# Optimization experiments

Measured on AMD Instinct MI355X. Metric: run time of the kernel, lower is better.

Reference implementation:

```python
import jax, jax.numpy as jnp
import numpy as np

NUM_HEADS = 8
EPS = 1e-5


def setup_inputs() -> dict:
    key = jax.random.key(0)
    ks = jax.random.split(key, 7)
    B, C, H, W, D = 1, 256, 16, 16, 16
    return {
        "x": jax.random.normal(ks[0], (B, C, H, W, D), dtype=jnp.float32),
        "w_dw": jax.random.normal(ks[1], (C, 1, 3, 3, 3), dtype=jnp.float32) * 0.05,
        "b_dw": jax.random.normal(ks[2], (C,), dtype=jnp.float32) * 0.05,
        "w_qkv": jax.random.normal(ks[3], (3 * C, C), dtype=jnp.float32) * 0.05,
        "b_qkv": jax.random.normal(ks[4], (3 * C,), dtype=jnp.float32) * 0.05,
        "w_proj": jax.random.normal(ks[5], (C, C), dtype=jnp.float32) * 0.05,
        "b_proj": jax.random.normal(ks[6], (C,), dtype=jnp.float32) * 0.05,
    }


def reference(x, w_dw, b_dw, w_qkv, b_qkv, w_proj, b_proj):
    B, C, H, W, D = x.shape
    nh = NUM_HEADS
    hd = C // nh
    scale = hd ** (-0.5)
    N = H * W * D

    # depthwise 3x3x3 conv (groups=C), SAME padding
    y = jax.lax.conv_general_dilated(
        x, w_dw, window_strides=(1, 1, 1), padding="SAME",
        dimension_numbers=("NCHWD", "OIHWD", "NCHWD"),
        feature_group_count=C,
    ) + b_dw[None, :, None, None, None]

    # InstanceNorm3d (affine=False): normalize over spatial dims per (b, c)
    mu = y.mean(axis=(2, 3, 4), keepdims=True)
    var = y.var(axis=(2, 3, 4), keepdims=True)
    y = (y - mu) * jax.lax.rsqrt(var + EPS)

    # 1x1x1 conv -> 3*C channels
    qkv = jnp.einsum("bchwd,oc->bohwd", y, w_qkv) + b_qkv[None, :, None, None, None]

    # [B, 3, nh, hd, N] -> q, k, v each [B, nh, N, hd]
    qkv = qkv.reshape(B, 3, nh, hd, N)
    q, k, v = jnp.transpose(qkv, (1, 0, 2, 4, 3))

    attn = jax.nn.softmax(jnp.einsum("bhnd,bhmd->bhnm", q, k) * scale, axis=-1)
    out = jnp.einsum("bhnm,bhmd->bhnd", attn, v)  # [B, nh, N, hd]

    # transpose(-1, -2) then reshape to [B, C, H, W, D]
    out = jnp.transpose(out, (0, 1, 3, 2)).reshape(B, C, H, W, D)

    # output 1x1x1 projection
    out = jnp.einsum("bchwd,oc->bohwd", out, w_proj) + b_proj[None, :, None, None, None]
    return out
```

## Files before the change

### kernel.cpp

```cpp
#include <hip/hip_runtime.h>
#include <hip/hip_bf16.h>

#define NSP 4096
#define QSC2 0.25503486f

typedef __attribute__((ext_vector_type(8))) short bf16x8;
typedef __attribute__((ext_vector_type(4))) float f32x4;
typedef __attribute__((ext_vector_type(16))) float f32x16;

__device__ __forceinline__ unsigned short f2bf(float f){
  union{float f;unsigned int u;}c; c.f=f;
  unsigned int r = c.u + 0x7fffu + ((c.u>>16)&1u);
  return (unsigned short)(r>>16);
}
__device__ __forceinline__ unsigned int pk2(float a, float b){
  __hip_bfloat162 p = __float22bfloat162_rn(make_float2(a, b));
  unsigned int r; __builtin_memcpy(&r, &p, 4); return r;
}
__device__ __forceinline__ ushort4 pk4(float a, float b, float c, float d){
  union { ushort4 u4; uint2 u2; } u;
  u.u2.x = pk2(a, b); u.u2.y = pk2(c, d);
  return u.u4;
}
__device__ __forceinline__ float bfu2f(unsigned short u){
  union { unsigned int i; float f; } c; c.i = ((unsigned int)u) << 16; return c.f;
}

__global__ __launch_bounds__(512) void k_dwconv(
    const float* __restrict__ x,
    const float* __restrict__ wdw,
    const float* __restrict__ bdw,
    unsigned short* __restrict__ ybn)
{
  const int c = blockIdx.x;
  const int tid = threadIdx.x;
  __shared__ float xs[4096];
  __shared__ float wsh[27];
  __shared__ float bsh;
  __shared__ float rs[8], rq[8];

  const float* xc = x + (size_t)c * NSP;
  for (int i = tid; i < 1024; i += 512) *(float4*)&xs[i*4] = ((const float4*)xc)[i];
  if (tid < 27) wsh[tid] = wdw[c*27 + tid];
  if (tid == 31) bsh = bdw[c];
  __syncthreads();

  float yv[8];
  float sum = 0.f, sumsq = 0.f;
  #pragma unroll
  for (int i = 0; i < 8; i++){
    const int n = (i << 9) + tid;
    const int h = n >> 8, w = (n >> 4) & 15, d = n & 15;
    float acc = bsh;
    #pragma unroll
    for (int kh = 0; kh < 3; kh++){
      const int hh = h + kh - 1;
      if ((unsigned)hh >= 16u) continue;
      #pragma unroll
      for (int kw = 0; kw < 3; kw++){
        const int ww = w + kw - 1;
        if ((unsigned)ww >= 16u) continue;
        #pragma unroll
        for (int kd = 0; kd < 3; kd++){
          const int dd = d + kd - 1;
          if ((unsigned)dd >= 16u) continue;
          acc += wsh[kh*9 + kw*3 + kd] * xs[(hh<<8) + (ww<<4) + dd];
        }
      }
    }
    yv[i] = acc; sum += acc; sumsq += acc*acc;
  }
  #pragma unroll
  for (int off = 32; off > 0; off >>= 1){
    sum   += __shfl_down(sum, off, 64);
    sumsq += __shfl_down(sumsq, off, 64);
  }
  const int wid = tid >> 6, lane = tid & 63;
  if (lane == 0){ rs[wid] = sum; rq[wid] = sumsq; }
  __syncthreads();
  float ts = 0.f, tq = 0.f;
  #pragma unroll
  for (int i = 0; i < 8; i++){ ts += rs[i]; tq += rq[i]; }
  const float mean = ts * (1.f/4096.f);
  const float var  = tq * (1.f/4096.f) - mean*mean;
  const float rinv = rsqrtf(var + 1e-5f);
  unsigned short* yo = ybn + (size_t)c * NSP;
  #pragma unroll
  for (int i = 0; i < 8; i++) yo[(i<<9) + tid] = f2bf((yv[i] - mean) * rinv);
}

__global__ __launch_bounds__(256) void k_trans(
    const unsigned short* __restrict__ ybn,
    unsigned short* __restrict__ ynT)
{
  __shared__ unsigned short T[64][72];
  const int tid = threadIdx.x;
  const int n0 = blockIdx.x * 64, c0 = blockIdx.y * 64;
  const int cl = tid >> 4, n4 = (tid & 15) * 4;
  #pragma unroll
  for (int i = 0; i < 4; i++){
    const int c = cl + i*16;
    const ushort4 v = *(const ushort4*)(ybn + (size_t)(c0 + c) * NSP + n0 + n4);
    T[n4+0][c] = v.x; T[n4+1][c] = v.y; T[n4+2][c] = v.z; T[n4+3][c] = v.w;
  }
  __syncthreads();
  const int nl = tid >> 2, s8 = (tid & 3) * 16;
  *(uint4*)(ynT + (size_t)(n0+nl)*256 + c0 + s8)     = *(const uint4*)&T[nl][s8];
  *(uint4*)(ynT + (size_t)(n0+nl)*256 + c0 + s8 + 8) = *(const uint4*)&T[nl][s8 + 8];
}

__global__ __launch_bounds__(256) void k_qkv(
    const float* __restrict__ wqkv,
    const float* __restrict__ bqkv,
    const unsigned short* __restrict__ ynT,
    unsigned short* __restrict__ qb, unsigned short* __restrict__ kb,
    unsigned short* __restrict__ vbt)
{
  __shared__ unsigned short Wb[64][264];
  const int tid = threadIdx.x;
  const int o0 = blockIdx.y * 64;
  const int n0 = blockIdx.x * 64;
  {
    const int row = tid & 63, part = tid >> 6;
    const float* src = wqkv + (size_t)(o0 + row) * 256 + part * 64;
    unsigned short* dst = &Wb[row][part*64];
    #pragma unroll
    for (int j = 0; j < 8; j++){
      const float4 a = ((const float4*)src)[2*j];
      const float4 b = ((const float4*)src)[2*j+1];
      *(ushort4*)&dst[j*8]     = pk4(a.x, a.y, a.z, a.w);
      *(ushort4*)&dst[j*8 + 4] = pk4(b.x, b.y, b.z, b.w);
    }
  }
  __syncthreads();

  const int w = tid >> 6, lane = tid & 63, quad = lane >> 4, cc = lane & 15;
  const int nbase = n0 + w*16;
  const bool isv = (o0 >= 512);
  f32x4 acc[4] = {};

  #pragma unroll
  for (int k = 0; k < 8; k++){
    const bf16x8 y0 = *(const bf16x8*)(ynT + (size_t)(nbase + cc) * 256 + k*32 + quad*8);
    #pragma unroll
    for (int os = 0; os < 4; os++){
      const bf16x8 wf = *(const bf16x8*)&Wb[os*16 + cc][k*32 + quad*8];
      if (!isv) acc[os] = __builtin_amdgcn_mfma_f32_16x16x32_bf16(y0, wf, acc[os], 0, 0, 0);
      else      acc[os] = __builtin_amdgcn_mfma_f32_16x16x32_bf16(wf, y0, acc[os], 0, 0, 0);
    }
  }

  if (!isv){
    #pragma unroll
    for (int os = 0; os < 4; os++){
      const int o = o0 + os*16 + cc;
      const int g = o >> 8, hh = (o >> 5) & 7, dd = o & 31;
      const float bias = bqkv[o];
      const float sc = (g == 0) ? QSC2 : 1.f;
      unsigned short* dst = (g == 0) ? qb : kb;
      #pragma unroll
      for (int r = 0; r < 4; r++){
        const int n = nbase + quad*4 + r;
        dst[((size_t)hh * NSP + n) * 32 + dd] = f2bf((acc[os][r] + bias) * sc);
      }
    }
  } else {
    #pragma unroll
    for (int os = 0; os < 4; os++){
      #pragma unroll
      for (int r = 0; r < 4; r++){
        const int orow = o0 - 512 + os*16 + quad*4 + r;
        const float bias = bqkv[512 + orow];
        const int n = nbase + cc;
        vbt[(size_t)orow * NSP + n] = f2bf(acc[os][r] + bias);
      }
    }
  }
}

__global__ __launch_bounds__(256) void k_attn(
    const unsigned short* __restrict__ qb,
    const unsigned short* __restrict__ kb,
    const unsigned short* __restrict__ vbt,
    unsigned short* __restrict__ opb, float* __restrict__ lp, int ktlen)
{
  const int h = blockIdx.y, q0 = blockIdx.x * 128, z = blockIdx.z;
  const int tid = threadIdx.x;
  const int w = tid >> 6, l = tid & 63;
  const int lq = l & 31, lb = l >> 5;

  __shared__ unsigned short ks [64][40];
  __shared__ unsigned short vsT[32][72];
  __shared__ unsigned short pst[128][72];

  const int qg = q0 + w*32 + lq;
  const bf16x8 qf0 = *(const bf16x8*)(qb + ((size_t)(h*NSP + qg))*32 + lb*8);
  const bf16x8 qf1 = *(const bf16x8*)(qb + ((size_t)(h*NSP + qg))*32 + 16 + lb*8);
  const unsigned short* kbase = kb  + (size_t)h * NSP * 32;
  const unsigned short* vbase = vbt + (size_t)h * 32 * NSP;

  f32x16 oacc = {};
  float lsum = 0.f;

  const int kt0 = z * ktlen;
  const int krow = tid >> 2, kseg = (tid & 3) * 8;
  const int vrow = tid >> 3, vseg = (tid & 7) * 8;
  const int iters = ktlen >> 6;

  for (int it = 0; it < iters; it++){
    const int kt = kt0 + it * 64;
    {
      *(uint4*)&ks[krow][kseg]  = *(const uint4*)(kbase + (size_t)(kt + krow) * 32 + kseg);
      *(uint4*)&vsT[vrow][vseg] = *(const uint4*)(vbase + (size_t)vrow * NSP + kt + vseg);
    }
    __syncthreads();

    #pragma unroll
    for (int t2 = 0; t2 < 2; t2++){
      const bf16x8 af0 = *(const bf16x8*)&ks[t2*32 + lq][lb*8];
      const bf16x8 af1 = *(const bf16x8*)&ks[t2*32 + lq][16 + lb*8];
      f32x16 sa = {};
      sa = __builtin_amdgcn_mfma_f32_32x32x16_bf16(af0, qf0, sa, 0, 0, 0);
      sa = __builtin_amdgcn_mfma_f32_32x32x16_bf16(af1, qf1, sa, 0, 0, 0);
      #pragma unroll
      for (int g = 0; g < 4; g++){
        const float p0 = __builtin_amdgcn_exp2f(sa[g*4+0]);
        const float p1 = __builtin_amdgcn_exp2f(sa[g*4+1]);
        const float p2 = __builtin_amdgcn_exp2f(sa[g*4+2]);
        const float p3 = __builtin_amdgcn_exp2f(sa[g*4+3]);
        lsum += (p0 + p1) + (p2 + p3);
        *(ushort4*)&pst[w*32 + lq][t2*32 + g*8 + lb*4] = pk4(p0, p1, p2, p3);
      }
    }
    #pragma unroll
    for (int ck = 0; ck < 4; ck++){
      const bf16x8 vf = *(const bf16x8*)&vsT[lq]       [ck*16 + lb*8];
      const bf16x8 pf = *(const bf16x8*)&pst[w*32 + lq][ck*16 + lb*8];
      oacc = __builtin_amdgcn_mfma_f32_32x32x16_bf16(vf, pf, oacc, 0, 0, 0);
    }
    __syncthreads();
  }

  lsum += __shfl_xor(lsum, 32, 64);

  unsigned short* dst = opb + ((size_t)z * NSP + qg) * 256 + h*32;
  #pragma unroll
  for (int g = 0; g < 4; g++){
    *(ushort4*)(dst + g*8 + lb*4) =
        pk4(oacc[g*4+0], oacc[g*4+1], oacc[g*4+2], oacc[g*4+3]);
  }
  if (lb == 0) lp[((size_t)z * 8 + h) * NSP + qg] = lsum;
}

__global__ __launch_bounds__(256) void k_proj(
    const float* __restrict__ wproj,
    const float* __restrict__ bproj,
    const unsigned short* __restrict__ opb,
    const float* __restrict__ lp,
    float* __restrict__ out, int nz)
{
  __shared__ unsigned short Wb[64][264];
  const int tid = threadIdx.x;
  const int o0 = blockIdx.y * 64;
  const int n0 = blockIdx.x * 64;
  {
    const int row = tid & 63, part = tid >> 6;
    const float* src = wproj + (size_t)(o0 + row) * 256 + part * 64;
    unsigned short* dst = &Wb[row][part*64];
    #pragma unroll
    for (int j = 0; j < 8; j++){
      const float4 a = ((const float4*)src)[2*j];
      const float4 b = ((const float4*)src)[2*j+1];
      *(ushort4*)&dst[j*8]     = pk4(a.x, a.y, a.z, a.w);
      *(ushort4*)&dst[j*8 + 4] = pk4(b.x, b.y, b.z, b.w);
    }
  }
  __syncthreads();

  const int w = tid >> 6, lane = tid & 63, quad = lane >> 4, cc = lane & 15;
  const int nr = n0 + w*16 + cc;
  f32x4 acc[4] = {};

  #pragma unroll
  for (int k = 0; k < 8; k++){
    float lt = 0.f;
    float s[8] = {};
    for (int z = 0; z < nz; z++){
      lt += lp[((size_t)z*8 + k) * NSP + nr];
      union { uint4 q; unsigned short u[8]; } v;
      v.q = *(const uint4*)(opb + ((size_t)z * NSP + nr) * 256 + k*32 + quad*8);
      #pragma unroll
      for (int j = 0; j < 8; j++) s[j] += bfu2f(v.u[j]);
    }
    const float r = 1.f / lt;
    union { bf16x8 v; ushort4 u[2]; } yb;
    yb.u[0] = pk4(s[0]*r, s[1]*r, s[2]*r, s[3]*r);
    yb.u[1] = pk4(s[4]*r, s[5]*r, s[6]*r, s[7]*r);
    #pragma unroll
    for (int os = 0; os < 4; os++){
      const bf16x8 wf = *(const bf16x8*)&Wb[os*16 + cc][k*32 + quad*8];
      acc[os] = __builtin_amdgcn_mfma_f32_16x16x32_bf16(wf, yb.v, acc[os], 0, 0, 0);
    }
  }

  #pragma unroll
  for (int os = 0; os < 4; os++){
    #pragma unroll
    for (int r = 0; r < 4; r++){
      const int o = o0 + os*16 + quad*4 + r;
      out[(size_t)o * NSP + nr] = acc[os][r] + bproj[o];
    }
  }
}

extern "C" void kernel_launch(void* const* d_in, const int* in_sizes, int n_in,
                              void* d_out, int out_size, void* d_ws, size_t ws_size,
                              hipStream_t stream) {
  (void)in_sizes; (void)n_in; (void)out_size;
  const float* x     = (const float*)d_in[0];
  const float* wdw   = (const float*)d_in[1];
  const float* bdw   = (const float*)d_in[2];
  const float* wqkv  = (const float*)d_in[3];
  const float* bqkv  = (const float*)d_in[4];
  const float* wproj = (const float*)d_in[5];
  const float* bproj = (const float*)d_in[6];
  float* out = (float*)d_out;

  const int nz = (ws_size >= ((size_t)16 << 20)) ? 4 : 2;
  const int ktlen = NSP / nz;

  char* ws = (char*)d_ws;
  const size_t opB = (size_t)nz << 21;
  unsigned short* opb = (unsigned short*)ws;
  unsigned short* ybn = (unsigned short*)ws;
  unsigned short* ynT = (unsigned short*)(ws + (2<<20));
  unsigned short* qb  = (unsigned short*)(ws + opB);
  unsigned short* kb  = (unsigned short*)(ws + opB + (2<<20));
  unsigned short* vbt = (unsigned short*)(ws + opB + (4<<20));
  float*          lp  = (float*)(ws + opB + (6<<20));

  k_dwconv <<<dim3(256),        dim3(512), 0, stream>>>(x, wdw, bdw, ybn);
  k_trans  <<<dim3(64, 4),      dim3(256), 0, stream>>>(ybn, ynT);
  k_qkv    <<<dim3(64, 12),     dim3(256), 0, stream>>>(wqkv, bqkv, ynT, qb, kb, vbt);
  k_attn   <<<dim3(32, 8, nz),  dim3(256), 0, stream>>>(qb, kb, vbt, opb, lp, ktlen);
  k_proj   <<<dim3(64, 4),      dim3(256), 0, stream>>>(wproj, bproj, opb, lp, out, nz);
}
```

Before: 145.6 us.

## Register-block dwconv, drop cancelled bias, vectorize qkv/proj epilogue stores

The depthwise conv now gives each thread 8 contiguous depth outputs computed from a sliding register window, in place of 8 strided points. This cuts shared-memory loads and boundary branches and makes the bf16 output store vectorized. The conv bias is removed because InstanceNorm subtracts the mean and cancels it. In the qkv and proj kernels the MFMA operands are swapped so each lane holds 4 contiguous outputs, which allows ushort4/float4 stores, and the qkv bias moves into shared memory. Exactness relies on bias cancellation, which is mathematically valid but shifts rounding slightly.

```diff
diff --git a/kernel.cpp b/kernel.cpp
--- a/kernel.cpp
+++ b/kernel.cpp
@@ -29,47 +29,55 @@
 __global__ __launch_bounds__(512) void k_dwconv(
     const float* __restrict__ x,
     const float* __restrict__ wdw,
-    const float* __restrict__ bdw,
     unsigned short* __restrict__ ybn)
 {
   const int c = blockIdx.x;
   const int tid = threadIdx.x;
   __shared__ float xs[4096];
   __shared__ float wsh[27];
-  __shared__ float bsh;
   __shared__ float rs[8], rq[8];
 
   const float* xc = x + (size_t)c * NSP;
-  for (int i = tid; i < 1024; i += 512) *(float4*)&xs[i*4] = ((const float4*)xc)[i];
+  {
+    const float4 a = ((const float4*)xc)[tid*2];
+    const float4 b = ((const float4*)xc)[tid*2 + 1];
+    *(float4*)&xs[tid*8]     = a;
+    *(float4*)&xs[tid*8 + 4] = b;
+  }
   if (tid < 27) wsh[tid] = wdw[c*27 + tid];
-  if (tid == 31) bsh = bdw[c];
-  __syncthreads();
-
-  float yv[8];
+  __syncthreads();
+
+  const int h = tid >> 5, w = (tid >> 1) & 15, d0 = (tid & 1) * 8;
+  float acc[8] = {};
+  #pragma unroll
+  for (int kh = 0; kh < 3; kh++){
+    const int hh = h + kh - 1;
+    if ((unsigned)hh >= 16u) continue;
+    #pragma unroll
+    for (int kw = 0; kw < 3; kw++){
+      const int ww = w + kw - 1;
+      if ((unsigned)ww >= 16u) continue;
+      const float* rowp = &xs[((hh << 4) + ww) << 4];
+      float win[10];
+      const float4 c0 = *(const float4*)&rowp[d0];
+      const float4 c1 = *(const float4*)&rowp[d0 + 4];
+      win[1] = c0.x; win[2] = c0.y; win[3] = c0.z; win[4] = c0.w;
+      win[5] = c1.x; win[6] = c1.y; win[7] = c1.z; win[8] = c1.w;
+      const float e7 = rowp[7], e8 = rowp[8];
+      win[0] = d0 ? e7 : 0.f;
+      win[9] = d0 ? 0.f : e8;
+      #pragma unroll
+      for (int kd = 0; kd < 3; kd++){
+        const float wv = wsh[kh*9 + kw*3 + kd];
+        #pragma unroll
+        for (int j = 0; j < 8; j++) acc[j] += wv * win[j + kd];
+      }
+    }
+  }
+
   float sum = 0.f, sumsq = 0.f;
   #pragma unroll
-  for (int i = 0; i < 8; i++){
-    const int n = (i << 9) + tid;
-    const int h = n >> 8, w = (n >> 4) & 15, d = n & 15;
-    float acc = bsh;
-    #pragma unroll
-    for (int kh = 0; kh < 3; kh++){
-      const int hh = h + kh - 1;
-      if ((unsigned)hh >= 16u) continue;
-      #pragma unroll
-      for (int kw = 0; kw < 3; kw++){
-        const int ww = w + kw - 1;
-        if ((unsigned)ww >= 16u) continue;
-        #pragma unroll
-        for (int kd = 0; kd < 3; kd++){
-          const int dd = d + kd - 1;
-          if ((unsigned)dd >= 16u) continue;
-          acc += wsh[kh*9 + kw*3 + kd] * xs[(hh<<8) + (ww<<4) + dd];
-        }
-      }
-    }
-    yv[i] = acc; sum += acc; sumsq += acc*acc;
-  }
+  for (int j = 0; j < 8; j++){ sum += acc[j]; sumsq += acc[j]*acc[j]; }
   #pragma unroll
   for (int off = 32; off > 0; off >>= 1){
     sum   += __shfl_down(sum, off, 64);
@@ -84,9 +92,12 @@
   const float mean = ts * (1.f/4096.f);
   const float var  = tq * (1.f/4096.f) - mean*mean;
   const float rinv = rsqrtf(var + 1e-5f);
-  unsigned short* yo = ybn + (size_t)c * NSP;
-  #pragma unroll
-  for (int i = 0; i < 8; i++) yo[(i<<9) + tid] = f2bf((yv[i] - mean) * rinv);
+
+  unsigned short* yo = ybn + (size_t)c * NSP + tid*8;
+  *(ushort4*)yo =
+      pk4((acc[0]-mean)*rinv, (acc[1]-mean)*rinv, (acc[2]-mean)*rinv, (acc[3]-mean)*rinv);
+  *(ushort4*)(yo + 4) =
+      pk4((acc[4]-mean)*rinv, (acc[5]-mean)*rinv, (acc[6]-mean)*rinv, (acc[7]-mean)*rinv);
 }
 
 __global__ __launch_bounds__(256) void k_trans(
@@ -117,6 +128,7 @@
     unsigned short* __restrict__ vbt)
 {
   __shared__ unsigned short Wb[64][264];
+  __shared__ float bsh[64];
   const int tid = threadIdx.x;
   const int o0 = blockIdx.y * 64;
   const int n0 = blockIdx.x * 64;
@@ -131,6 +143,7 @@
       *(ushort4*)&dst[j*8]     = pk4(a.x, a.y, a.z, a.w);
       *(ushort4*)&dst[j*8 + 4] = pk4(b.x, b.y, b.z, b.w);
     }
+    if (tid < 64) bsh[tid] = bqkv[o0 + tid];
   }
   __syncthreads();
 
@@ -145,35 +158,32 @@
     #pragma unroll
     for (int os = 0; os < 4; os++){
       const bf16x8 wf = *(const bf16x8*)&Wb[os*16 + cc][k*32 + quad*8];
-      if (!isv) acc[os] = __builtin_amdgcn_mfma_f32_16x16x32_bf16(y0, wf, acc[os], 0, 0, 0);
-      else      acc[os] = __builtin_amdgcn_mfma_f32_16x16x32_bf16(wf, y0, acc[os], 0, 0, 0);
+      if (!isv) acc[os] = __builtin_amdgcn_mfma_f32_16x16x32_bf16(wf, y0, acc[os], 0, 0, 0);
+      else      acc[os] = __builtin_amdgcn_mfma_f32_16x16x32_bf16(y0, wf, acc[os], 0, 0, 0);
     }
   }
 
   if (!isv){
     #pragma unroll
     for (int os = 0; os < 4; os++){
-      const int o = o0 + os*16 + cc;
-      const int g = o >> 8, hh = (o >> 5) & 7, dd = o & 31;
-      const float bias = bqkv[o];
+      const int obase = o0 + os*16 + quad*4;
+      const int g = obase >> 8, hh = (obase >> 5) & 7, dd0 = obase & 31;
+      const int n = nbase + cc;
+      unsigned short* dst = (g == 0) ? qb : kb;
       const float sc = (g == 0) ? QSC2 : 1.f;
-      unsigned short* dst = (g == 0) ? qb : kb;
-      #pragma unroll
-      for (int r = 0; r < 4; r++){
-        const int n = nbase + quad*4 + r;
-        dst[((size_t)hh * NSP + n) * 32 + dd] = f2bf((acc[os][r] + bias) * sc);
-      }
+      const int bb = os*16 + quad*4;
+      *(ushort4*)&dst[((size_t)hh * NSP + n) * 32 + dd0] =
+          pk4((acc[os][0] + bsh[bb+0]) * sc, (acc[os][1] + bsh[bb+1]) * sc,
+              (acc[os][2] + bsh[bb+2]) * sc, (acc[os][3] + bsh[bb+3]) * sc);
     }
   } else {
     #pragma unroll
     for (int os = 0; os < 4; os++){
-      #pragma unroll
-      for (int r = 0; r < 4; r++){
-        const int orow = o0 - 512 + os*16 + quad*4 + r;
-        const float bias = bqkv[512 + orow];
-        const int n = nbase + cc;
-        vbt[(size_t)orow * NSP + n] = f2bf(acc[os][r] + bias);
-      }
+      const int orow = o0 - 512 + os*16 + cc;
+      const float bias = bsh[os*16 + cc];
+      const int n4 = nbase + quad*4;
+      *(ushort4*)&vbt[(size_t)orow * NSP + n4] =
+          pk4(acc[os][0] + bias, acc[os][1] + bias, acc[os][2] + bias, acc[os][3] + bias);
     }
   }
 }
@@ -278,7 +288,8 @@
   __syncthreads();
 
   const int w = tid >> 6, lane = tid & 63, quad = lane >> 4, cc = lane & 15;
-  const int nr = n0 + w*16 + cc;
+  const int nbase = n0 + w*16;
+  const int nr = nbase + cc;
   f32x4 acc[4] = {};
 
   #pragma unroll
@@ -299,17 +310,18 @@
     #pragma unroll
     for (int os = 0; os < 4; os++){
       const bf16x8 wf = *(const bf16x8*)&Wb[os*16 + cc][k*32 + quad*8];
-      acc[os] = __builtin_amdgcn_mfma_f32_16x16x32_bf16(wf, yb.v, acc[os], 0, 0, 0);
+      acc[os] = __builtin_amdgcn_mfma_f32_16x16x32_bf16(yb.v, wf, acc[os], 0, 0, 0);
     }
   }
 
   #pragma unroll
   for (int os = 0; os < 4; os++){
-    #pragma unroll
-    for (int r = 0; r < 4; r++){
-      const int o = o0 + os*16 + quad*4 + r;
-      out[(size_t)o * NSP + nr] = acc[os][r] + bproj[o];
-    }
+    const int o = o0 + os*16 + cc;
+    const float bias = bproj[o];
+    const int n4 = nbase + quad*4;
+    *(float4*)&out[(size_t)o * NSP + n4] =
+        make_float4(acc[os][0] + bias, acc[os][1] + bias,
+                    acc[os][2] + bias, acc[os][3] + bias);
   }
 }
 
@@ -319,7 +331,7 @@
   (void)in_sizes; (void)n_in; (void)out_size;
   const float* x     = (const float*)d_in[0];
   const float* wdw   = (const float*)d_in[1];
-  const float* bdw   = (const float*)d_in[2];
+  const float* bdw   = (const float*)d_in[2];  (void)bdw;
   const float* wqkv  = (const float*)d_in[3];
   const float* bqkv  = (const float*)d_in[4];
   const float* wproj = (const float*)d_in[5];
@@ -339,7 +351,7 @@
   unsigned short* vbt = (unsigned short*)(ws + opB + (4<<20));
   float*          lp  = (float*)(ws + opB + (6<<20));
 
-  k_dwconv <<<dim3(256),        dim3(512), 0, stream>>>(x, wdw, bdw, ybn);
+  k_dwconv <<<dim3(256),        dim3(512), 0, stream>>>(x, wdw, ybn);
   k_trans  <<<dim3(64, 4),      dim3(256), 0, stream>>>(ybn, ynT);
   k_qkv    <<<dim3(64, 12),     dim3(256), 0, stream>>>(wqkv, bqkv, ynT, qb, kb, vbt);
   k_attn   <<<dim3(32, 8, nz),  dim3(256), 0, stream>>>(qb, kb, vbt, opb, lp, ktlen);
```

New measurement: 145.5 us. Within noise of the previous version (-0.0%).
